# Kernel optimization log

Hardware: AMD Instinct MI355X
Metric: run time of the kernel (lower is better)

The kernel has to match this reference:

```python
import jax, jax.numpy as jnp
import numpy as np

N_HEADS = 16
NEG_INF = -1e9


def setup_inputs() -> dict:
    key = jax.random.key(0)
    ks = jax.random.split(key, 8)
    B, S, D = 2, 2048, 1024
    HD = D // N_HEADS
    x = jax.random.normal(ks[0], (B, S, D), dtype=jnp.float32)
    # RoPE frequencies (llama-style): theta = 10000^(-2i/head_dim)
    inv_freq = 1.0 / (10000.0 ** (np.arange(0, HD, 2, dtype=np.float32) / HD))  # [HD//2]
    angles = np.arange(S, dtype=np.float32)[:, None] * inv_freq[None, :]        # [S, HD//2]
    freqs_cos = jnp.asarray(np.cos(angles))
    freqs_sin = jnp.asarray(np.sin(angles))
    # additive causal mask [1,1,S,S]
    mask = jnp.where(np.tril(np.ones((S, S), dtype=bool)), 0.0, NEG_INF).astype(jnp.float32)[None, None]
    scale = 0.02
    wq = jax.random.normal(ks[1], (D, D), dtype=jnp.float32) * scale
    wk = jax.random.normal(ks[2], (D, D), dtype=jnp.float32) * scale
    wv = jax.random.normal(ks[3], (D, D), dtype=jnp.float32) * scale
    wo = jax.random.normal(ks[4], (D, D), dtype=jnp.float32) * scale
    return {"x": x, "freqs_cos": freqs_cos, "freqs_sin": freqs_sin, "mask": mask,
            "wq": wq, "wk": wk, "wv": wv, "wo": wo}


def _rope(t, cos, sin):
    # t: [B,S,H,HD]; cos/sin: [S,HD//2]; complex mult (t0 + i t1) * (cos + i sin)
    b, s, h, hd = t.shape
    tr = t.reshape(b, s, h, hd // 2, 2)
    t0, t1 = tr[..., 0], tr[..., 1]
    c = cos[None, :, None, :]
    sn = sin[None, :, None, :]
    out = jnp.stack([t0 * c - t1 * sn, t0 * sn + t1 * c], axis=-1)
    return out.reshape(b, s, h, hd)


def reference(x, freqs_cos, freqs_sin, mask, wq, wk, wv, wo):
    b, s, d = x.shape
    hd = d // N_HEADS
    # torch Linear: y = x @ W.T
    xq = (x @ wq.T).reshape(b, s, N_HEADS, hd)
    xk = (x @ wk.T).reshape(b, s, N_HEADS, hd)
    xv = (x @ wv.T).reshape(b, s, N_HEADS, hd)
    xq = _rope(xq, freqs_cos, freqs_sin)
    xk = _rope(xk, freqs_cos, freqs_sin)
    # [B,H,S,S] scores
    scores = jnp.einsum('bqhd,bkhd->bhqk', xq, xk) / jnp.sqrt(jnp.asarray(hd, x.dtype))
    scores = scores + mask
    probs = jax.nn.softmax(scores.astype(jnp.float32), axis=-1).astype(x.dtype)
    out = jnp.einsum('bhqk,bkhd->bqhd', probs, xv).reshape(b, s, d)
    return out @ wo.T
```

## Files before the change

kernel.cpp:

```cpp
#include <hip/hip_runtime.h>
#include <hip/hip_bf16.h>
#include <cstdint>

typedef __attribute__((ext_vector_type(4))) float f32x4;
typedef __attribute__((ext_vector_type(8))) short s16x8;
typedef __attribute__((ext_vector_type(4))) unsigned short u16x4;
typedef unsigned short u16;
typedef unsigned int u32;
typedef unsigned long long u64;

__device__ __forceinline__ float b2f(u16 u){ u32 v = ((u32)u)<<16; return __builtin_bit_cast(float, v); }
__device__ __forceinline__ u16 f2b(float f){
  __hip_bfloat16 h = __float2bfloat16(f);
  return __builtin_bit_cast(u16, h);
}

__device__ __forceinline__ void gld16(const void* g, void* l){
  __builtin_amdgcn_global_load_lds((const __attribute__((address_space(1))) void*)g,
                                   (__attribute__((address_space(3))) void*)l, 16, 0, 0);
}

__device__ __forceinline__ f32x4 mfma16(s16x8 a, s16x8 b, f32x4 c){
  return __builtin_amdgcn_mfma_f32_16x16x32_bf16(a, b, c, 0, 0, 0);
}

#define WS_XB   0u
#define WS_WQ   (4u<<20)
#define WS_WK   (5u<<20)
#define WS_WV   (6u<<20)
#define WS_WO   (7u<<20)
#define WS_Q    (8u<<20)
#define WS_K    (12u<<20)
#define WS_VT   (16u<<20)
#define WS_AO   (20u<<20)

#define QSCALE 0.18033688f

__global__ __launch_bounds__(256) void k_convert(const float* __restrict__ x,
    const float* __restrict__ wq, const float* __restrict__ wk,
    const float* __restrict__ wv, const float* __restrict__ wo,
    u16* __restrict__ ws){
  u32 idx = blockIdx.x*256u + threadIdx.x;
  const float* src; u16* dst;
  if (idx < (1u<<20)) { src = x + (u64)idx*4u; dst = ws + WS_XB + (u64)idx*4u; }
  else {
    u32 widx = idx - (1u<<20);
    u32 wsel = widx >> 18;
    u32 off  = (widx & ((1u<<18)-1u)) * 4u;
    const float* sp = (wsel==0u)?wq:(wsel==1u)?wk:(wsel==2u)?wv:wo;
    src = sp + off; dst = ws + WS_WQ + (u64)wsel*(1u<<20) + off;
  }
  f32x4 v = *(const f32x4*)src;
  u16x4 o = { f2b(v[0]), f2b(v[1]), f2b(v[2]), f2b(v[3]) };
  *(u16x4*)dst = o;
}

__global__ __launch_bounds__(256,3) void k_gemm(u16* __restrict__ ws, float* __restrict__ out,
    const float* __restrict__ fc, const float* __restrict__ fs, int pass){
  __shared__ char sm[32768];
  const u32 tid = threadIdx.x;
  const u32 w = tid>>6, l = tid&63u, g = l>>4, li = l&15u;
  const u32 wr = w>>1, wc = w&1u;
  u32 bx = blockIdx.x;

  const u16 *Ap, *Bp; u32 arow0, brow0; int mode;
  if (pass == 0) {
    u32 seg = bx >> 8, b2 = bx & 255u;
    if (seg < 2u) {
      Ap = ws + WS_XB; Bp = ws + (seg ? WS_WK : WS_WQ);
      arow0 = (b2 >> 3) * 128u; brow0 = (b2 & 7u) * 128u; mode = (int)seg;
    } else {
      Ap = ws + WS_WV; Bp = ws + WS_XB;
      arow0 = (b2 >> 5) * 128u; brow0 = (b2 & 31u) * 128u; mode = 2;
    }
  } else {
    Ap = ws + WS_AO; Bp = ws + WS_WO;
    arow0 = (bx >> 3) * 128u; brow0 = (bx & 7u) * 128u; mode = 3;
  }

  f32x4 acc[4][4];
  #pragma unroll
  for (u32 m=0;m<4;++m)
    #pragma unroll
    for (u32 n=0;n<4;++n) acc[m][n] = 0.0f;

  for (u32 t = 0; t < 16u; ++t) {
    const u32 k0 = t*64u;
    #pragma unroll
    for (u32 j = 0; j < 4u; ++j) {
      u32 p = w*4096u + j*1024u + l*16u;
      u32 row = p >> 7, colb = p & 127u;
      u32 cS = colb ^ ((row & 7u) << 4);
      gld16(Ap + (u64)(arow0 + row)*1024u + k0 + (cS>>1), sm + w*4096u + j*1024u);
      gld16(Bp + (u64)(brow0 + row)*1024u + k0 + (cS>>1), sm + 16384u + w*4096u + j*1024u);
    }
    __syncthreads();
    s16x8 af[2][4], bf[2][4];
    #pragma unroll
    for (u32 kk=0;kk<2u;++kk){
      #pragma unroll
      for (u32 m=0;m<4;++m){
        u32 row = wr*64u + m*16u + li;
        af[kk][m] = *(const s16x8*)(sm + row*128u + ((kk*64u + g*16u) ^ ((row&7u)<<4)));
      }
      #pragma unroll
      for (u32 n=0;n<4;++n){
        u32 row = wc*64u + n*16u + li;
        bf[kk][n] = *(const s16x8*)(sm + 16384u + row*128u + ((kk*64u + g*16u) ^ ((row&7u)<<4)));
      }
    }
    #pragma unroll
    for (u32 kk=0;kk<2u;++kk)
      #pragma unroll
      for (u32 m=0;m<4;++m)
        #pragma unroll
        for (u32 n=0;n<4;++n)
          acc[m][n] = mfma16(af[kk][m], bf[kk][n], acc[m][n]);
    __syncthreads();
  }

  u16* qdst = ws + WS_Q; u16* kdst = ws + WS_K; u16* vtd = ws + WS_VT;
  if (mode <= 1) {
    #pragma unroll
    for (u32 m=0;m<4;++m)
      #pragma unroll
      for (u32 n=0;n<4;++n)
        #pragma unroll
        for (u32 q=0;q<4;++q){
          u32 row = wr*64u + m*16u + 4u*g + q;
          u32 colb = (wc*64u + n*16u + li)*2u;
          *(u16*)(sm + row*256u + (colb ^ ((row&7u)<<4))) = f2b(acc[m][n][q]);
        }
    __syncthreads();
    u32 row = tid >> 1, half = tid & 1u;
    u32 r = arow0 + row;
    u32 b = r >> 11, s = r & 2047u;
    u32 h = (brow0 >> 6) + half;
    float qs = (mode==0) ? QSCALE : 1.0f;
    u16* d = ((mode==0) ? qdst : kdst) + (u64)(((b<<4)+h)*2048u + s)*64u;
    #pragma unroll
    for (u32 u0=0; u0<8u; ++u0){
      s16x8 cv = *(const s16x8*)(sm + row*256u + ((half*128u + u0*16u) ^ ((row&7u)<<4)));
      f32x4 cvv = *(const f32x4*)(fc + s*32u + u0*4u);
      f32x4 svv = *(const f32x4*)(fs + s*32u + u0*4u);
      s16x8 o;
      #pragma unroll
      for (u32 i=0;i<4;++i){
        float t0 = b2f((u16)cv[2*i]), t1 = b2f((u16)cv[2*i+1]);
        o[2*i]   = (short)f2b((t0*cvv[i] - t1*svv[i])*qs);
        o[2*i+1] = (short)f2b((t0*svv[i] + t1*cvv[i])*qs);
      }
      *(s16x8*)(d + u0*8u) = o;
    }
  } else {
    #pragma unroll
    for (u32 m=0;m<4;++m){
      u32 r0 = arow0 + wr*64u + m*16u + 4u*g;
      #pragma unroll
      for (u32 n=0;n<4;++n){
        u32 c = brow0 + wc*64u + n*16u + li;
        #pragma unroll
        for (u32 q=0;q<4;++q){
          float v = acc[m][n][q];
          u32 r = r0 + q;
          if (mode == 2) vtd[(u64)r*4096u + c] = f2b(v);
          else           out[(u64)r*1024u + c] = v;
        }
      }
    }
  }
}

__global__ __launch_bounds__(256) void k_attn(u16* __restrict__ ws){
  __shared__ char sm[25600];
  const u32 tid = threadIdx.x;
  const u32 w = tid>>6, l = tid&63u, g = l>>4, li = l&15u;
  u32 bx = blockIdx.x;
  u32 qt = 31u - (bx >> 5);
  u32 bh = bx & 31u;
  u32 b = bh >> 4, h = bh & 15u;
  const u16* Q  = ws + WS_Q + (u64)bh*2048u*64u;
  const u16* Kp = ws + WS_K + (u64)bh*2048u*64u;
  const u16* Vt = ws + WS_VT + (u64)(h*64u)*4096u + b*2048u;
  u16* AO = ws + WS_AO;
  const u32 qbase = qt*64u;
  const u32 qw = qbase + w*16u;

  s16x8 qa[2];
  #pragma unroll
  for (u32 kk=0;kk<2;++kk)
    qa[kk] = *(const s16x8*)(Q + (u64)(qw + li)*64u + kk*32u + g*8u);

  s16x8 ones;
  #pragma unroll
  for (u32 i=0;i<8;++i) ones[i] = (short)0x3F80;

  f32x4 o[4]; f32x4 lsum;
  #pragma unroll
  for (u32 n=0;n<4;++n) o[n] = 0.0f;
  lsum = 0.0f;

  char* pl = sm + 16384 + w*2304u;
  const u32 nt = qt + 1u;
  for (u32 t = 0; t < nt; ++t) {
    const u32 kvb = t*64u;
    #pragma unroll
    for (u32 j=0;j<2u;++j){
      u32 p = (w*2u+j)*1024u + l*16u;
      u32 row = p >> 7, colb = p & 127u;
      u32 cS = colb ^ ((row & 7u) << 4);
      gld16(Kp + (u64)(kvb + row)*64u + (cS>>1), sm + (w*2u+j)*1024u);
      gld16(Vt + (u64)row*4096u + kvb + (cS>>1), sm + 8192u + (w*2u+j)*1024u);
    }
    __syncthreads();

    f32x4 sv[4];
    #pragma unroll
    for (u32 n=0;n<4;++n) sv[n] = 0.0f;
    #pragma unroll
    for (u32 n=0;n<4;++n){
      u32 kvr = n*16u + li;
      #pragma unroll
      for (u32 kk=0;kk<2u;++kk){
        s16x8 kf = *(const s16x8*)(sm + kvr*128u + ((kk*64u + g*16u) ^ ((kvr&7u)<<4)));
        sv[n] = mfma16(qa[kk], kf, sv[n]);
      }
    }
    if (t == nt - 1u) {
      #pragma unroll
      for (u32 n=0;n<4;++n)
        #pragma unroll
        for (u32 q=0;q<4;++q){
          u32 qr = qw + 4u*g + q;
          u32 kc = kvb + n*16u + li;
          if (kc > qr) sv[n][q] = -1e9f;
        }
    }
    #pragma unroll
    for (u32 n=0;n<4;++n)
      #pragma unroll
      for (u32 q=0;q<4;++q)
        *(u16*)(pl + (4u*g + q)*144u + (n*16u + li)*2u) = f2b(exp2f(sv[n][q]));
    #pragma unroll
    for (u32 kk=0;kk<2u;++kk){
      s16x8 pa = *(const s16x8*)(pl + li*144u + kk*64u + g*16u);
      lsum = mfma16(pa, ones, lsum);
      #pragma unroll
      for (u32 n=0;n<4;++n){
        u32 hr = n*16u + li;
        s16x8 vf = *(const s16x8*)(sm + 8192u + hr*128u + ((kk*64u + g*16u) ^ ((hr&7u)<<4)));
        o[n] = mfma16(pa, vf, o[n]);
      }
    }
    __syncthreads();
  }

  #pragma unroll
  for (u32 q=0;q<4;++q){
    float inv = 1.0f / lsum[q];
    u32 qr = qw + 4u*g + q;
    #pragma unroll
    for (u32 n=0;n<4;++n){
      u32 hd = n*16u + li;
      AO[((u64)(b*2048u + qr))*1024u + h*64u + hd] = f2b(o[n][q] * inv);
    }
  }
}

extern "C" void kernel_launch(void* const* d_in, const int* in_sizes, int n_in,
                              void* d_out, int out_size, void* d_ws, size_t ws_size,
                              hipStream_t stream) {
  const float* x  = (const float*)d_in[0];
  const float* fc = (const float*)d_in[1];
  const float* fs = (const float*)d_in[2];
  const float* wq = (const float*)d_in[4];
  const float* wk = (const float*)d_in[5];
  const float* wv = (const float*)d_in[6];
  const float* wo = (const float*)d_in[7];
  u16* ws = (u16*)d_ws;
  float* out = (float*)d_out;

  k_convert<<<8192, 256, 0, stream>>>(x, wq, wk, wv, wo, ws);
  k_gemm  <<<768,  256, 0, stream>>>(ws, out, fc, fs, 0);
  k_attn  <<<1024, 256, 0, stream>>>(ws);
  k_gemm  <<<256,  256, 0, stream>>>(ws, out, fc, fs, 1);
}
```

Before: 119.8 us.

## Double-buffer K/V tiles and process 128 query rows per attention block

The attention kernel now gives each wave 32 query rows (two MFMA row tiles) instead of 16, so each K/V fragment read from LDS feeds two MFMAs, and the grid is halved to 512 blocks. K/V tiles are double-buffered in shared memory so the next tile's global-to-LDS load is issued before the current tile is computed. Waves skip fully masked tiles, and the causal query-tile order is interleaved to balance work across blocks. The cost is twice the LDS and more accumulator registers, which may reduce occupancy.

New measurement: 130.2 us. 8.7% more time.

```diff
diff --git a/kernel.cpp b/kernel.cpp
--- a/kernel.cpp
+++ b/kernel.cpp
@@ -172,99 +172,131 @@
 }
 
 __global__ __launch_bounds__(256) void k_attn(u16* __restrict__ ws){
-  __shared__ char sm[25600];
+  __shared__ char sm[51200];
   const u32 tid = threadIdx.x;
   const u32 w = tid>>6, l = tid&63u, g = l>>4, li = l&15u;
   u32 bx = blockIdx.x;
-  u32 qt = 31u - (bx >> 5);
+  u32 k5 = bx >> 5;
+  u32 qt = (k5 < 8u) ? (15u - 2u*k5) : (2u*k5 - 16u);
   u32 bh = bx & 31u;
   u32 b = bh >> 4, h = bh & 15u;
   const u16* Q  = ws + WS_Q + (u64)bh*2048u*64u;
   const u16* Kp = ws + WS_K + (u64)bh*2048u*64u;
   const u16* Vt = ws + WS_VT + (u64)(h*64u)*4096u + b*2048u;
   u16* AO = ws + WS_AO;
-  const u32 qbase = qt*64u;
-  const u32 qw = qbase + w*16u;
-
-  s16x8 qa[2];
-  #pragma unroll
-  for (u32 kk=0;kk<2;++kk)
-    qa[kk] = *(const s16x8*)(Q + (u64)(qw + li)*64u + kk*32u + g*8u);
+  const u32 qw = qt*128u + w*32u;
+
+  s16x8 qa[2][2];
+  #pragma unroll
+  for (u32 m=0;m<2;++m)
+    #pragma unroll
+    for (u32 kk=0;kk<2;++kk)
+      qa[m][kk] = *(const s16x8*)(Q + (u64)(qw + m*16u + li)*64u + kk*32u + g*8u);
 
   s16x8 ones;
   #pragma unroll
   for (u32 i=0;i<8;++i) ones[i] = (short)0x3F80;
 
-  f32x4 o[4]; f32x4 lsum;
-  #pragma unroll
-  for (u32 n=0;n<4;++n) o[n] = 0.0f;
-  lsum = 0.0f;
-
-  char* pl = sm + 16384 + w*2304u;
-  const u32 nt = qt + 1u;
-  for (u32 t = 0; t < nt; ++t) {
-    const u32 kvb = t*64u;
+  f32x4 o[2][4]; f32x4 lsum[2];
+  #pragma unroll
+  for (u32 m=0;m<2;++m){
+    #pragma unroll
+    for (u32 n=0;n<4;++n) o[m][n] = 0.0f;
+    lsum[m] = 0.0f;
+  }
+
+  char* pl = sm + 32768 + w*4608u;
+  const u32 nt = qt*2u + 2u;
+
+  auto STAGE = [&](u32 cb, u32 kvb){
     #pragma unroll
     for (u32 j=0;j<2u;++j){
       u32 p = (w*2u+j)*1024u + l*16u;
       u32 row = p >> 7, colb = p & 127u;
       u32 cS = colb ^ ((row & 7u) << 4);
-      gld16(Kp + (u64)(kvb + row)*64u + (cS>>1), sm + (w*2u+j)*1024u);
-      gld16(Vt + (u64)row*4096u + kvb + (cS>>1), sm + 8192u + (w*2u+j)*1024u);
+      gld16(Kp + (u64)(kvb + row)*64u + (cS>>1), sm + cb + (w*2u+j)*1024u);
+      gld16(Vt + (u64)row*4096u + kvb + (cS>>1), sm + 16384u + cb + (w*2u+j)*1024u);
+    }
+  };
+
+  STAGE(0u, 0u);
+  __syncthreads();
+
+  u32 cur = 0u;
+  for (u32 t = 0; t < nt; ++t) {
+    const u32 kvb = t*64u;
+    if (t + 1u < nt) STAGE((cur^1u)*8192u, kvb + 64u);
+    if (kvb <= qw + 31u) {
+      const u32 cb = cur*8192u;
+      f32x4 sv[2][4];
+      #pragma unroll
+      for (u32 m=0;m<2;++m)
+        #pragma unroll
+        for (u32 n=0;n<4;++n) sv[m][n] = 0.0f;
+      #pragma unroll
+      for (u32 n=0;n<4;++n){
+        u32 kvr = n*16u + li;
+        #pragma unroll
+        for (u32 kk=0;kk<2u;++kk){
+          s16x8 kf = *(const s16x8*)(sm + cb + kvr*128u + ((kk*64u + g*16u) ^ ((kvr&7u)<<4)));
+          #pragma unroll
+          for (u32 m=0;m<2;++m)
+            sv[m][n] = mfma16(qa[m][kk], kf, sv[m][n]);
+        }
+      }
+      if (kvb + 63u > qw) {
+        #pragma unroll
+        for (u32 m=0;m<2;++m)
+          #pragma unroll
+          for (u32 n=0;n<4;++n)
+            #pragma unroll
+            for (u32 q=0;q<4;++q){
+              u32 qr = qw + m*16u + 4u*g + q;
+              u32 kc = kvb + n*16u + li;
+              if (kc > qr) sv[m][n][q] = -1e9f;
+            }
+      }
+      #pragma unroll
+      for (u32 m=0;m<2;++m)
+        #pragma unroll
+        for (u32 n=0;n<4;++n)
+          #pragma unroll
+          for (u32 q=0;q<4;++q)
+            *(u16*)(pl + (m*16u + 4u*g + q)*144u + (n*16u + li)*2u) = f2b(exp2f(sv[m][n][q]));
+      #pragma unroll
+      for (u32 kk=0;kk<2u;++kk){
+        s16x8 pa[2];
+        #pragma unroll
+        for (u32 m=0;m<2;++m){
+          pa[m] = *(const s16x8*)(pl + (m*16u + li)*144u + kk*64u + g*16u);
+          lsum[m] = mfma16(pa[m], ones, lsum[m]);
+        }
+        #pragma unroll
+        for (u32 n=0;n<4;++n){
+          u32 hr = n*16u + li;
+          s16x8 vf = *(const s16x8*)(sm + 16384u + cb + hr*128u + ((kk*64u + g*16u) ^ ((hr&7u)<<4)));
+          #pragma unroll
+          for (u32 m=0;m<2;++m)
+            o[m][n] = mfma16(pa[m], vf, o[m][n]);
+        }
+      }
     }
     __syncthreads();
-
-    f32x4 sv[4];
-    #pragma unroll
-    for (u32 n=0;n<4;++n) sv[n] = 0.0f;
-    #pragma unroll
-    for (u32 n=0;n<4;++n){
-      u32 kvr = n*16u + li;
-      #pragma unroll
-      for (u32 kk=0;kk<2u;++kk){
-        s16x8 kf = *(const s16x8*)(sm + kvr*128u + ((kk*64u + g*16u) ^ ((kvr&7u)<<4)));
-        sv[n] = mfma16(qa[kk], kf, sv[n]);
-      }
-    }
-    if (t == nt - 1u) {
-      #pragma unroll
-      for (u32 n=0;n<4;++n)
-        #pragma unroll
-        for (u32 q=0;q<4;++q){
-          u32 qr = qw + 4u*g + q;
-          u32 kc = kvb + n*16u + li;
-          if (kc > qr) sv[n][q] = -1e9f;
-        }
-    }
-    #pragma unroll
-    for (u32 n=0;n<4;++n)
-      #pragma unroll
-      for (u32 q=0;q<4;++q)
-        *(u16*)(pl + (4u*g + q)*144u + (n*16u + li)*2u) = f2b(exp2f(sv[n][q]));
-    #pragma unroll
-    for (u32 kk=0;kk<2u;++kk){
-      s16x8 pa = *(const s16x8*)(pl + li*144u + kk*64u + g*16u);
-      lsum = mfma16(pa, ones, lsum);
+    cur ^= 1u;
+  }
+
+  #pragma unroll
+  for (u32 m=0;m<2;++m)
+    #pragma unroll
+    for (u32 q=0;q<4;++q){
+      float inv = 1.0f / lsum[m][q];
+      u32 qr = qw + m*16u + 4u*g + q;
       #pragma unroll
       for (u32 n=0;n<4;++n){
-        u32 hr = n*16u + li;
-        s16x8 vf = *(const s16x8*)(sm + 8192u + hr*128u + ((kk*64u + g*16u) ^ ((hr&7u)<<4)));
-        o[n] = mfma16(pa, vf, o[n]);
-      }
-    }
-    __syncthreads();
-  }
-
-  #pragma unroll
-  for (u32 q=0;q<4;++q){
-    float inv = 1.0f / lsum[q];
-    u32 qr = qw + 4u*g + q;
-    #pragma unroll
-    for (u32 n=0;n<4;++n){
-      u32 hd = n*16u + li;
-      AO[((u64)(b*2048u + qr))*1024u + h*64u + hd] = f2b(o[n][q] * inv);
-    }
-  }
+        u32 hd = n*16u + li;
+        AO[((u64)(b*2048u + qr))*1024u + h*64u + hd] = f2b(o[m][n][q] * inv);
+      }
+    }
 }
 
 extern "C" void kernel_launch(void* const* d_in, const int* in_sizes, int n_in,
@@ -282,6 +314,6 @@
 
   k_convert<<<8192, 256, 0, stream>>>(x, wq, wk, wv, wo, ws);
   k_gemm  <<<768,  256, 0, stream>>>(ws, out, fc, fs, 0);
-  k_attn  <<<1024, 256, 0, stream>>>(ws);
+  k_attn  <<<512,  256, 0, stream>>>(ws);
   k_gemm  <<<256,  256, 0, stream>>>(ws, out, fc, fs, 1);
 }
```

## Double-buffer LDS tiles in GEMM and attention kernels to overlap loads

Applied to the files above, without the earlier changes.

Both the projection GEMM and the attention kernel now split shared memory into two stage buffers. The global-to-LDS load of the next K-tile (GEMM) or K/V tile (attention) is issued before the MFMA work on the current one. This leaves one barrier per iteration and is meant to hide global memory latency behind compute. In exchange, shared memory use doubles (64KB for the GEMM, about 41KB for attention) and the GEMM launch-bounds occupancy hint drops from 3 to 2 blocks, which may reduce latency hiding across waves.

Measured after the change: 108.3 us. 9.6% less time.

```diff
diff --git a/kernel.cpp b/kernel.cpp
--- a/kernel.cpp
+++ b/kernel.cpp
@@ -55,9 +55,9 @@
   *(u16x4*)dst = o;
 }
 
-__global__ __launch_bounds__(256,3) void k_gemm(u16* __restrict__ ws, float* __restrict__ out,
+__global__ __launch_bounds__(256,2) void k_gemm(u16* __restrict__ ws, float* __restrict__ out,
     const float* __restrict__ fc, const float* __restrict__ fs, int pass){
-  __shared__ char sm[32768];
+  __shared__ char sm[65536];
   const u32 tid = threadIdx.x;
   const u32 w = tid>>6, l = tid&63u, g = l>>4, li = l&15u;
   const u32 wr = w>>1, wc = w&1u;
@@ -84,29 +84,37 @@
     #pragma unroll
     for (u32 n=0;n<4;++n) acc[m][n] = 0.0f;
 
-  for (u32 t = 0; t < 16u; ++t) {
+  auto STAGE_G = [&](u32 s, u32 t){
     const u32 k0 = t*64u;
     #pragma unroll
     for (u32 j = 0; j < 4u; ++j) {
       u32 p = w*4096u + j*1024u + l*16u;
       u32 row = p >> 7, colb = p & 127u;
       u32 cS = colb ^ ((row & 7u) << 4);
-      gld16(Ap + (u64)(arow0 + row)*1024u + k0 + (cS>>1), sm + w*4096u + j*1024u);
-      gld16(Bp + (u64)(brow0 + row)*1024u + k0 + (cS>>1), sm + 16384u + w*4096u + j*1024u);
-    }
-    __syncthreads();
+      gld16(Ap + (u64)(arow0 + row)*1024u + k0 + (cS>>1), sm + s*32768u + w*4096u + j*1024u);
+      gld16(Bp + (u64)(brow0 + row)*1024u + k0 + (cS>>1), sm + s*32768u + 16384u + w*4096u + j*1024u);
+    }
+  };
+
+  STAGE_G(0u, 0u);
+  __syncthreads();
+
+  u32 cur = 0u;
+  for (u32 t = 0; t < 16u; ++t) {
+    if (t + 1u < 16u) STAGE_G(cur^1u, t+1u);
+    const u32 cb = cur*32768u;
     s16x8 af[2][4], bf[2][4];
     #pragma unroll
     for (u32 kk=0;kk<2u;++kk){
       #pragma unroll
       for (u32 m=0;m<4;++m){
         u32 row = wr*64u + m*16u + li;
-        af[kk][m] = *(const s16x8*)(sm + row*128u + ((kk*64u + g*16u) ^ ((row&7u)<<4)));
+        af[kk][m] = *(const s16x8*)(sm + cb + row*128u + ((kk*64u + g*16u) ^ ((row&7u)<<4)));
       }
       #pragma unroll
       for (u32 n=0;n<4;++n){
         u32 row = wc*64u + n*16u + li;
-        bf[kk][n] = *(const s16x8*)(sm + 16384u + row*128u + ((kk*64u + g*16u) ^ ((row&7u)<<4)));
+        bf[kk][n] = *(const s16x8*)(sm + cb + 16384u + row*128u + ((kk*64u + g*16u) ^ ((row&7u)<<4)));
       }
     }
     #pragma unroll
@@ -117,6 +125,7 @@
         for (u32 n=0;n<4;++n)
           acc[m][n] = mfma16(af[kk][m], bf[kk][n], acc[m][n]);
     __syncthreads();
+    cur ^= 1u;
   }
 
   u16* qdst = ws + WS_Q; u16* kdst = ws + WS_K; u16* vtd = ws + WS_VT;
@@ -172,7 +181,7 @@
 }
 
 __global__ __launch_bounds__(256) void k_attn(u16* __restrict__ ws){
-  __shared__ char sm[25600];
+  __shared__ char sm[41984];
   const u32 tid = threadIdx.x;
   const u32 w = tid>>6, l = tid&63u, g = l>>4, li = l&15u;
   u32 bx = blockIdx.x;
@@ -183,8 +192,7 @@
   const u16* Kp = ws + WS_K + (u64)bh*2048u*64u;
   const u16* Vt = ws + WS_VT + (u64)(h*64u)*4096u + b*2048u;
   u16* AO = ws + WS_AO;
-  const u32 qbase = qt*64u;
-  const u32 qw = qbase + w*16u;
+  const u32 qw = qt*64u + w*16u;
 
   s16x8 qa[2];
   #pragma unroll
@@ -200,19 +208,28 @@
   for (u32 n=0;n<4;++n) o[n] = 0.0f;
   lsum = 0.0f;
 
-  char* pl = sm + 16384 + w*2304u;
+  char* pl = sm + 32768 + w*2304u;
   const u32 nt = qt + 1u;
-  for (u32 t = 0; t < nt; ++t) {
-    const u32 kvb = t*64u;
+
+  auto STAGE = [&](u32 s, u32 kvb){
     #pragma unroll
     for (u32 j=0;j<2u;++j){
       u32 p = (w*2u+j)*1024u + l*16u;
       u32 row = p >> 7, colb = p & 127u;
       u32 cS = colb ^ ((row & 7u) << 4);
-      gld16(Kp + (u64)(kvb + row)*64u + (cS>>1), sm + (w*2u+j)*1024u);
-      gld16(Vt + (u64)row*4096u + kvb + (cS>>1), sm + 8192u + (w*2u+j)*1024u);
-    }
-    __syncthreads();
+      gld16(Kp + (u64)(kvb + row)*64u + (cS>>1), sm + s*16384u + (w*2u+j)*1024u);
+      gld16(Vt + (u64)row*4096u + kvb + (cS>>1), sm + s*16384u + 8192u + (w*2u+j)*1024u);
+    }
+  };
+
+  STAGE(0u, 0u);
+  __syncthreads();
+
+  u32 cur = 0u;
+  for (u32 t = 0; t < nt; ++t) {
+    const u32 kvb = t*64u;
+    if (t + 1u < nt) STAGE(cur^1u, kvb + 64u);
+    const u32 cb = cur*16384u;
 
     f32x4 sv[4];
     #pragma unroll
@@ -222,7 +239,7 @@
       u32 kvr = n*16u + li;
       #pragma unroll
       for (u32 kk=0;kk<2u;++kk){
-        s16x8 kf = *(const s16x8*)(sm + kvr*128u + ((kk*64u + g*16u) ^ ((kvr&7u)<<4)));
+        s16x8 kf = *(const s16x8*)(sm + cb + kvr*128u + ((kk*64u + g*16u) ^ ((kvr&7u)<<4)));
         sv[n] = mfma16(qa[kk], kf, sv[n]);
       }
     }
@@ -248,11 +265,12 @@
       #pragma unroll
       for (u32 n=0;n<4;++n){
         u32 hr = n*16u + li;
-        s16x8 vf = *(const s16x8*)(sm + 8192u + hr*128u + ((kk*64u + g*16u) ^ ((hr&7u)<<4)));
+        s16x8 vf = *(const s16x8*)(sm + cb + 8192u + hr*128u + ((kk*64u + g*16u) ^ ((hr&7u)<<4)));
         o[n] = mfma16(pa, vf, o[n]);
       }
     }
     __syncthreads();
+    cur ^= 1u;
   }
 
   #pragma unroll
```
